# Kernel optimization log

Measured on AMD Instinct MI355X. Metric: run time of the kernel, lower is better.

Reference implementation:

```python
import jax, jax.numpy as jnp
import numpy as np

NG, NPG, EPG = 64, 256, 2048        # graphs, nodes/graph, edges/graph
N, E = NG * NPG, NG * EPG
FN, FE, FG = 256, 64, 128           # node/edge/global feature dims
MSG_DIMS = [FE + 2 * FN + FG, 512, 512, 256]   # message_arch '512-512-256'
UPD_DIMS = [256 + FN + FG, 512, 256]           # node_arch '512-256'
N_EMB_G, OUT_NODE, OUT_ACT = 256, 64, 8


def _mlp(x, params):
    # Linear -> ReLU stack (Dropout is identity in eval mode)
    for w, b in params:
        x = jax.nn.relu(x @ w + b)
    return x


def setup_inputs():
    key = jax.random.key(0)
    ks = jax.random.split(key, 24)
    nodes = jax.random.normal(ks[0], (N, FN), jnp.float32)
    edge_attr = jax.random.normal(ks[1], (E, FE), jnp.float32)
    global_attr = jax.random.normal(ks[2], (NG, FG), jnp.float32)
    # edges are grouped by graph (matches repeat_interleave(global, num_edges))
    rng = np.random.default_rng(0)
    gid_e = np.repeat(np.arange(NG), EPG)
    src = gid_e * NPG + rng.integers(0, NPG, E)
    tgt = gid_e * NPG + rng.integers(0, NPG, E)
    edge_indices = jnp.asarray(np.stack([src, tgt]), jnp.int32)
    num_nodes = jnp.full((NG,), NPG, jnp.int32)
    num_edges = jnp.full((NG,), EPG, jnp.int32)
    batch_indices = jnp.asarray(np.repeat(np.arange(NG), NPG), jnp.int32)

    def lin(k, fi, fo):
        kw, kb = jax.random.split(k)
        lim = 1.0 / np.sqrt(fi)
        return (jax.random.uniform(kw, (fi, fo), jnp.float32, -lim, lim),
                jax.random.uniform(kb, (fo,), jnp.float32, -lim, lim))

    inp = dict(nodes=nodes, edge_attr=edge_attr, global_attr=global_attr,
               edge_indices=edge_indices, num_nodes=num_nodes,
               num_edges=num_edges, batch_indices=batch_indices)
    for i in range(3):
        w, b = lin(ks[3 + i], MSG_DIMS[i], MSG_DIMS[i + 1])
        inp[f'msg_w{i}'], inp[f'msg_b{i}'] = w, b
    for i in range(2):
        w, b = lin(ks[6 + i], UPD_DIMS[i], UPD_DIMS[i + 1])
        inp[f'upd_w{i}'], inp[f'upd_b{i}'] = w, b
    inp['glob_w'], inp['glob_b'] = lin(ks[8], UPD_DIMS[-1] + FG, N_EMB_G)
    inp['emb_w'], inp['emb_b'] = lin(ks[9], UPD_DIMS[-1], OUT_NODE)
    inp['act_w'], inp['act_b'] = lin(ks[10], N_EMB_G, OUT_ACT)
    return inp


def reference(nodes, edge_attr, global_attr, edge_indices, num_nodes,
              num_edges, batch_indices, msg_w0, msg_b0, msg_w1, msg_b1,
              msg_w2, msg_b2, upd_w0, upd_b0, upd_w1, upd_b1,
              glob_w, glob_b, emb_w, emb_b, act_w, act_b):
    n, e = nodes.shape[0], edge_indices.shape[1]
    ng = global_attr.shape[0]
    src, tgt = edge_indices[0], edge_indices[1]
    glob_e = jnp.repeat(global_attr, num_edges, axis=0, total_repeat_length=e)
    concat = jnp.concatenate([nodes[src], edge_attr, nodes[tgt], glob_e], axis=1)
    # message_nn ends with ReLU; outer F.relu is a no-op on non-neg values
    message = _mlp(concat, [(msg_w0, msg_b0), (msg_w1, msg_b1), (msg_w2, msg_b2)])
    # scatter_max into per-node slots; messages >= 0 so zeros init matches fill=0
    aggr = jnp.zeros((n, message.shape[1]), message.dtype).at[tgt].max(message)
    glob_n = jnp.repeat(global_attr, num_nodes, axis=0, total_repeat_length=n)
    h = _mlp(jnp.concatenate([nodes, aggr, glob_n], axis=1),
             [(upd_w0, upd_b0), (upd_w1, upd_b1)])
    agg_nodes = jnp.zeros((ng, h.shape[1]), h.dtype).at[batch_indices].max(h)
    g = jax.nn.relu(jnp.concatenate([agg_nodes, global_attr], axis=1) @ glob_w + glob_b)
    node_pred = jax.nn.relu(h @ emb_w + emb_b)
    action = jax.nn.softmax(g @ act_w + act_b, axis=1)
    return node_pred, action
```

## Files before the change

kernel.cpp:

```cpp
#include <hip/hip_runtime.h>
#include <hip/hip_bf16.h>

typedef unsigned short u16;
using u16x4 = __attribute__((ext_vector_type(4))) unsigned short;
using u16x8 = __attribute__((ext_vector_type(8))) unsigned short;
using u32x4 = __attribute__((ext_vector_type(4))) unsigned int;
using f32x4 = __attribute__((ext_vector_type(4))) float;
using bf16x8 = __attribute__((ext_vector_type(8))) __bf16;

#define TNG 64
#define TNN 16384
#define TNE 131072
#define TFN 256
#define TFE 64
#define TFG 128

__device__ __forceinline__ u16 f2bf(float f) {
    unsigned u = __float_as_uint(f);
    unsigned r = (u + 0x7FFFu + ((u >> 16) & 1u)) >> 16;
    return (u16)r;
}
__device__ __forceinline__ float b2f(u16 h) {
    return __uint_as_float(((unsigned)h) << 16);
}

__device__ __forceinline__ void gload_lds16(const u16* g, u16* l) {
    __builtin_amdgcn_global_load_lds(
        (const __attribute__((address_space(1))) void*)g,
        (__attribute__((address_space(3))) void*)l, 16, 0, 0);
}

__device__ __forceinline__ int xcd_swz(int bid, int nwg) {
    return (nwg & 7) == 0 ? (bid & 7) * (nwg >> 3) + (bid >> 3) : bid;
}


__global__ void cast_kernel(const float* __restrict__ in, u16* __restrict__ out, int n4) {
    int i = blockIdx.x * 256 + threadIdx.x;
    if (i >= n4) return;
    f32x4 v = *(const f32x4*)(in + (size_t)i * 4);
    u16x4 o;
    o.x = f2bf(v.x); o.y = f2bf(v.y); o.z = f2bf(v.z); o.w = f2bf(v.w);
    *(u16x4*)(out + (size_t)i * 4) = o;
}


struct PrepTab {
    const float* W[8];
    int out_off[8];
    int Nin[8], Nact[8], r0[8], Ksub[8];
    int tile0[8];
    int tkn[8];
};

__global__ __launch_bounds__(256) void prep_weights_kernel(PrepTab tab, u16* __restrict__ wsbase) {
    const int b = blockIdx.x;
    int i = 7;
#pragma unroll
    for (int j = 7; j > 0; --j)
        if (b < tab.tile0[j]) i = j - 1;
    const int loc = b - tab.tile0[i];
    const int tk = loc % tab.tkn[i];
    const int tn = loc / tab.tkn[i];
    const int kb = tk * 64, nb = tn * 64;
    const int Nin = tab.Nin[i], Nact = tab.Nact[i], r0 = tab.r0[i], Ksub = tab.Ksub[i];
    const float* W = tab.W[i];
    u16* outp = wsbase + tab.out_off[i];

    __shared__ float t[64][65];
    const int tid = threadIdx.x;
    const int nl = tid & 63;
    const bool nok = (nb + nl) < Nact;
#pragma unroll 4
    for (int kk = tid >> 6; kk < 64; kk += 4) {
        float v = nok ? W[(size_t)(r0 + kb + kk) * Nin + nb + nl] : 0.0f;
        t[kk][nl] = v;
    }
    __syncthreads();
    const int kl = tid & 63;
#pragma unroll 4
    for (int nn = tid >> 6; nn < 64; nn += 4)
        outp[(size_t)(nb + nn) * Ksub + kb + kl] = f2bf(t[kl][nn]);
}


template <int K, int NXSH, bool RELU, bool OUT_BF16>
__global__ __launch_bounds__(256) void gemm_bt_kernel(
    const u16* __restrict__ A, const u16* __restrict__ Bt,
    const float* __restrict__ bias, void* __restrict__ Cv,
    int Nout, int ldc) {
    constexpr int NT = K / 32;
    __shared__ u16 As[3][4096];
    __shared__ u16 Bs[3][4096];
    const int w = xcd_swz(blockIdx.x, gridDim.x);
    const int bxi = w & ((1 << NXSH) - 1);
    const int byi = w >> NXSH;
    const int tid = threadIdx.x;
    const int wave = tid >> 6, lane = tid & 63;
    const int wr = wave >> 1, wc = wave & 1;
    const size_t brow = (size_t)byi * 128;
    const size_t bcol = (size_t)bxi * 128;
    const int srow = tid >> 2;
    const int qsrc = (tid & 3) ^ ((srow >> 1) & 3);
    const u16* aSrc = A + (brow + srow) * (size_t)K + qsrc * 8;
    const u16* bSrc = Bt + (bcol + srow) * (size_t)K + qsrc * 8;
    const size_t stepRows = (size_t)64 * K;

    auto stage = [&](int t, int buf) {
        const int k0 = t * 32;
        gload_lds16(aSrc + k0, &As[buf][tid * 8]);
        gload_lds16(aSrc + stepRows + k0, &As[buf][tid * 8 + 2048]);
        gload_lds16(bSrc + k0, &Bs[buf][tid * 8]);
        gload_lds16(bSrc + stepRows + k0, &Bs[buf][tid * 8 + 2048]);
    };

    f32x4 acc[4][4] = {};

    stage(0, 0);
    stage(1, 1);
#pragma unroll
    for (int t = 0; t < NT; ++t) {
        const int cur = t % 3;
        if (t + 1 < NT) asm volatile("s_waitcnt vmcnt(4)" ::: "memory");
        else            asm volatile("s_waitcnt vmcnt(0)" ::: "memory");
        __builtin_amdgcn_s_barrier();
        if (t + 2 < NT) stage(t + 2, (t + 2) % 3);
        bf16x8 af[4], bfv[4];
#pragma unroll
        for (int m = 0; m < 4; ++m) {
            const int row = wr * 64 + m * 16 + (lane & 15);
            const int slot = (lane >> 4) ^ ((row >> 1) & 3);
            af[m] = *(const bf16x8*)&As[cur][row * 32 + slot * 8];
        }
#pragma unroll
        for (int n = 0; n < 4; ++n) {
            const int row = wc * 64 + n * 16 + (lane & 15);
            const int slot = (lane >> 4) ^ ((row >> 1) & 3);
            bfv[n] = *(const bf16x8*)&Bs[cur][row * 32 + slot * 8];
        }
#pragma unroll
        for (int m = 0; m < 4; ++m)
#pragma unroll
            for (int n = 0; n < 4; ++n)
                acc[m][n] = __builtin_amdgcn_mfma_f32_16x16x32_bf16(af[m], bfv[n], acc[m][n], 0, 0, 0);
    }

    const int rowSub = wr * 64 + (lane >> 4) * 4;
#pragma unroll
    for (int n = 0; n < 4; ++n) {
        const int col = (int)bcol + wc * 64 + n * 16 + (lane & 15);
        if (col >= Nout) continue;
        const float bv = bias ? bias[col] : 0.0f;
#pragma unroll
        for (int m = 0; m < 4; ++m) {
#pragma unroll
            for (int i = 0; i < 4; ++i) {
                float v = acc[m][n][i] + bv;
                if (RELU) v = fmaxf(v, 0.0f);
                size_t off = (brow + rowSub + m * 16 + i) * (size_t)ldc + col;
                if (OUT_BF16) ((u16*)Cv)[off] = f2bf(v);
                else ((float*)Cv)[off] = v;
            }
        }
    }
}


__global__ __launch_bounds__(256) void gemm_u0_kernel(
    const u16* __restrict__ nodes_bf, const u16* __restrict__ aggr,
    const u16* __restrict__ glob_bf, const u16* __restrict__ U0T,
    const float* __restrict__ bias, u16* __restrict__ C) {
    constexpr int NT = 20;
    __shared__ u16 As[3][4096];
    __shared__ u16 Bs[3][4096];
    const int w = xcd_swz(blockIdx.x, gridDim.x);
    const int bxi = w & 3;
    const int byi = w >> 2;
    const int tid = threadIdx.x;
    const int wave = tid >> 6, lane = tid & 63;
    const int wr = wave >> 1, wc = wave & 1;
    const size_t brow = (size_t)byi * 128;
    const size_t bcol = (size_t)bxi * 128;
    const int srow = tid >> 2;
    const int scol = ((tid & 3) ^ ((srow >> 1) & 3)) * 8;
    const int r0i = (int)brow + srow;
    const u16* bSrc = U0T + (bcol + srow) * (size_t)640 + scol;

    auto stage = [&](int t, int buf) {
        const int k0 = t * 32;
        const u16 *p0, *p1;
        if (k0 < 256) {
            p0 = nodes_bf + (size_t)r0i * 256 + k0 + scol;
            p1 = nodes_bf + (size_t)(r0i + 64) * 256 + k0 + scol;
        } else if (k0 < 512) {
            p0 = aggr + (size_t)r0i * 256 + (k0 - 256) + scol;
            p1 = aggr + (size_t)(r0i + 64) * 256 + (k0 - 256) + scol;
        } else {
            p0 = glob_bf + (size_t)(r0i >> 8) * 128 + (k0 - 512) + scol;
            p1 = glob_bf + (size_t)((r0i + 64) >> 8) * 128 + (k0 - 512) + scol;
        }
        gload_lds16(p0, &As[buf][tid * 8]);
        gload_lds16(p1, &As[buf][tid * 8 + 2048]);
        gload_lds16(bSrc + k0, &Bs[buf][tid * 8]);
        gload_lds16(bSrc + (size_t)64 * 640 + k0, &Bs[buf][tid * 8 + 2048]);
    };

    f32x4 acc[4][4] = {};

    stage(0, 0);
    stage(1, 1);
#pragma unroll
    for (int t = 0; t < NT; ++t) {
        const int cur = t % 3;
        if (t + 1 < NT) asm volatile("s_waitcnt vmcnt(4)" ::: "memory");
        else            asm volatile("s_waitcnt vmcnt(0)" ::: "memory");
        __builtin_amdgcn_s_barrier();
        if (t + 2 < NT) stage(t + 2, (t + 2) % 3);
        bf16x8 af[4], bfv[4];
#pragma unroll
        for (int m = 0; m < 4; ++m) {
            const int row = wr * 64 + m * 16 + (lane & 15);
            const int slot = (lane >> 4) ^ ((row >> 1) & 3);
            af[m] = *(const bf16x8*)&As[cur][row * 32 + slot * 8];
        }
#pragma unroll
        for (int n = 0; n < 4; ++n) {
            const int row = wc * 64 + n * 16 + (lane & 15);
            const int slot = (lane >> 4) ^ ((row >> 1) & 3);
            bfv[n] = *(const bf16x8*)&Bs[cur][row * 32 + slot * 8];
        }
#pragma unroll
        for (int m = 0; m < 4; ++m)
#pragma unroll
            for (int n = 0; n < 4; ++n)
                acc[m][n] = __builtin_amdgcn_mfma_f32_16x16x32_bf16(af[m], bfv[n], acc[m][n], 0, 0, 0);
    }

    const int rowSub = wr * 64 + (lane >> 4) * 4;
#pragma unroll
    for (int n = 0; n < 4; ++n) {
        const int col = (int)bcol + wc * 64 + n * 16 + (lane & 15);
        const float bv = bias[col];
#pragma unroll
        for (int m = 0; m < 4; ++m)
#pragma unroll
            for (int i = 0; i < 4; ++i) {
                float v = fmaxf(acc[m][n][i] + bv, 0.0f);
                C[(brow + rowSub + m * 16 + i) * (size_t)512 + col] = f2bf(v);
            }
    }
}


__global__ __launch_bounds__(256) void gd_kernel(const float* __restrict__ glob,
                                                 const float* __restrict__ msg_w0,
                                                 const float* __restrict__ b0,
                                                 float* __restrict__ Gdb,
                                                 u16* __restrict__ glob_bf) {
    int g = blockIdx.x;
    __shared__ float in[TFG];
    if (threadIdx.x < TFG) {
        float v = glob[g * TFG + threadIdx.x];
        in[threadIdx.x] = v;
        glob_bf[g * TFG + threadIdx.x] = f2bf(v);
    }
    __syncthreads();
    for (int j = threadIdx.x; j < 512; j += 256) {
        float s = b0[j];
        for (int k = 0; k < TFG; ++k) s += in[k] * msg_w0[(size_t)(576 + k) * 512 + j];
        Gdb[(size_t)g * 512 + j] = s;
    }
}


__global__ __launch_bounds__(256) void h1_fused_kernel(
    const float* __restrict__ Ef, const u16* __restrict__ WbT,
    const u16* __restrict__ Pac, const float* __restrict__ Gdb,
    const int* __restrict__ src, const int* __restrict__ tgt,
    u16* __restrict__ h1, int e0) {
    __shared__ u16 smem[17408];
    u16* As = smem;
    u16* Bs = smem + 8192;
    const int w = xcd_swz(blockIdx.x, gridDim.x);
    const int bxi = w & 3;
    const int byi = w >> 2;
    const int tid = threadIdx.x;
    const int wave = tid >> 6, lane = tid & 63;
    const int wr = wave >> 1, wc = wave & 1;
    const int brow = byi * 128;
    const int bcol = bxi * 128;

    {
        const int r = tid >> 2;
        const int cq = (tid & 3) * 2;
        const int sw = r & 7;
#pragma unroll
        for (int h = 0; h < 2; ++h) {
            const float* sp = Ef + (size_t)(e0 + brow + r + h * 64) * 64 + cq * 8;
            f32x4 v0 = *(const f32x4*)(sp);
            f32x4 v1 = *(const f32x4*)(sp + 4);
            f32x4 v2 = *(const f32x4*)(sp + 8);
            f32x4 v3 = *(const f32x4*)(sp + 12);
            u16x8 o0, o1;
            o0[0] = f2bf(v0.x); o0[1] = f2bf(v0.y); o0[2] = f2bf(v0.z); o0[3] = f2bf(v0.w);
            o0[4] = f2bf(v1.x); o0[5] = f2bf(v1.y); o0[6] = f2bf(v1.z); o0[7] = f2bf(v1.w);
            o1[0] = f2bf(v2.x); o1[1] = f2bf(v2.y); o1[2] = f2bf(v2.z); o1[3] = f2bf(v2.w);
            o1[4] = f2bf(v3.x); o1[5] = f2bf(v3.y); o1[6] = f2bf(v3.z); o1[7] = f2bf(v3.w);
            *(u16x8*)&As[(r + h * 64) * 64 + (cq ^ sw) * 8] = o0;
            *(u16x8*)&As[(r + h * 64) * 64 + ((cq + 1) ^ sw) * 8] = o1;
        }
#pragma unroll
        for (int j = 0; j < 4; ++j) {
            int li = j * 256 + tid;
            int row = li >> 3;
            int gslot = (li & 7) ^ (row & 7);
            gload_lds16(WbT + (size_t)(bcol + row) * 64 + gslot * 8, &Bs[li * 8]);
        }
    }
    __syncthreads();

    f32x4 acc[4][4] = {};
#pragma unroll
    for (int k0 = 0; k0 < 64; k0 += 32) {
        bf16x8 af[4], bv[4];
#pragma unroll
        for (int m = 0; m < 4; ++m) {
            const int row = wr * 64 + m * 16 + (lane & 15);
            const int slot = ((k0 >> 3) + (lane >> 4)) ^ (row & 7);
            af[m] = *(const bf16x8*)&As[row * 64 + slot * 8];
        }
#pragma unroll
        for (int n = 0; n < 4; ++n) {
            const int row = wc * 64 + n * 16 + (lane & 15);
            const int slot = ((k0 >> 3) + (lane >> 4)) ^ (row & 7);
            bv[n] = *(const bf16x8*)&Bs[row * 64 + slot * 8];
        }
#pragma unroll
        for (int m = 0; m < 4; ++m)
#pragma unroll
            for (int n = 0; n < 4; ++n)
                acc[m][n] = __builtin_amdgcn_mfma_f32_16x16x32_bf16(af[m], bv[n], acc[m][n], 0, 0, 0);
    }
    __syncthreads();

    const int rowSub = wr * 64 + (lane >> 4) * 4;
#pragma unroll
    for (int m = 0; m < 4; ++m)
#pragma unroll
        for (int n = 0; n < 4; ++n)
#pragma unroll
            for (int i = 0; i < 4; ++i)
                smem[(rowSub + m * 16 + i) * 136 + wc * 64 + n * 16 + (lane & 15)] =
                    f2bf(acc[m][n][i]);
    __syncthreads();

#pragma unroll
    for (int it = 0; it < 8; ++it) {
        int lin = it * 256 + tid;
        int r = lin >> 4;
        int q = (lin & 15) * 8;
        int e = e0 + brow + r;
        int s = src[e];
        int t = tgt[e];
        int g = e >> 11;
        int col = bcol + q;
        u16x8 pa = *(const u16x8*)(Pac + (size_t)s * 1024 + col);
        u16x8 pc = *(const u16x8*)(Pac + (size_t)t * 1024 + 512 + col);
        u16x8 eb = *(const u16x8*)&smem[r * 136 + q];
        f32x4 g0 = *(const f32x4*)(Gdb + (size_t)g * 512 + col);
        f32x4 g1 = *(const f32x4*)(Gdb + (size_t)g * 512 + col + 4);
        u16x8 o;
#pragma unroll
        for (int j = 0; j < 8; ++j) {
            float gd = (j < 4) ? g0[j] : g1[j - 4];
            float v = b2f(pa[j]) + b2f(pc[j]) + b2f(eb[j]) + gd;
            o[j] = f2bf(fmaxf(v, 0.0f));
        }
        *(u16x8*)(h1 + (size_t)(brow + r) * 512 + col) = o;
    }
}


__global__ __launch_bounds__(1024) void scatter_max_kernel(
    const u16* __restrict__ msg, const int* __restrict__ tgt,
    u16* __restrict__ aggr) {
    int g = blockIdx.x >> 2;
    int fc = blockIdx.x & 3;
    __shared__ unsigned smax[256 * 64];
    int tid = threadIdx.x;
    for (int i = tid; i < 256 * 64; i += 1024) smax[i] = 0u;
    __syncthreads();
    const int eg = g * 2048;
    const int n0 = g * 256;
    const int f4 = (tid & 15) * 4;
    const int elane = tid >> 4;
    const u16* mbase = msg + fc * 64 + f4;
#pragma unroll
    for (int wv = 0; wv < 32; wv += 4) {
        const int e = eg + elane + wv * 64;
        int t0 = tgt[e], t1 = tgt[e + 64], t2 = tgt[e + 128], t3 = tgt[e + 192];
        u16x4 m0 = *(const u16x4*)(mbase + (size_t)e * 256);
        u16x4 m1 = *(const u16x4*)(mbase + (size_t)(e + 64) * 256);
        u16x4 m2 = *(const u16x4*)(mbase + (size_t)(e + 128) * 256);
        u16x4 m3 = *(const u16x4*)(mbase + (size_t)(e + 192) * 256);
        int a0 = t0 - n0, a1 = t1 - n0, a2 = t2 - n0, a3 = t3 - n0;
        if ((unsigned)a0 < 256u) {
            atomicMax(&smax[a0 * 64 + f4],     ((unsigned)m0.x) << 16);
            atomicMax(&smax[a0 * 64 + f4 + 1], ((unsigned)m0.y) << 16);
            atomicMax(&smax[a0 * 64 + f4 + 2], ((unsigned)m0.z) << 16);
            atomicMax(&smax[a0 * 64 + f4 + 3], ((unsigned)m0.w) << 16);
        }
        if ((unsigned)a1 < 256u) {
            atomicMax(&smax[a1 * 64 + f4],     ((unsigned)m1.x) << 16);
            atomicMax(&smax[a1 * 64 + f4 + 1], ((unsigned)m1.y) << 16);
            atomicMax(&smax[a1 * 64 + f4 + 2], ((unsigned)m1.z) << 16);
            atomicMax(&smax[a1 * 64 + f4 + 3], ((unsigned)m1.w) << 16);
        }
        if ((unsigned)a2 < 256u) {
            atomicMax(&smax[a2 * 64 + f4],     ((unsigned)m2.x) << 16);
            atomicMax(&smax[a2 * 64 + f4 + 1], ((unsigned)m2.y) << 16);
            atomicMax(&smax[a2 * 64 + f4 + 2], ((unsigned)m2.z) << 16);
            atomicMax(&smax[a2 * 64 + f4 + 3], ((unsigned)m2.w) << 16);
        }
        if ((unsigned)a3 < 256u) {
            atomicMax(&smax[a3 * 64 + f4],     ((unsigned)m3.x) << 16);
            atomicMax(&smax[a3 * 64 + f4 + 1], ((unsigned)m3.y) << 16);
            atomicMax(&smax[a3 * 64 + f4 + 2], ((unsigned)m3.z) << 16);
            atomicMax(&smax[a3 * 64 + f4 + 3], ((unsigned)m3.w) << 16);
        }
    }
    __syncthreads();
    for (int i = tid; i < 256 * 64; i += 1024) {
        int nl = i >> 6, ff = i & 63;
        aggr[(size_t)(n0 + nl) * 256 + fc * 64 + ff] = (u16)(smax[nl * 64 + ff] >> 16);
    }
}


__global__ __launch_bounds__(256) void head_kernel(
    const u16* __restrict__ h, const float* __restrict__ glob,
    const float* __restrict__ W, const float* __restrict__ b,
    const float* __restrict__ actw, const float* __restrict__ actb,
    float* __restrict__ out_act) {
    int g = blockIdx.x;
    int tid = threadIdx.x;
    __shared__ float in[384];
    __shared__ float go[256];
    __shared__ float logits[8];
    {
        const size_t base = (size_t)g * 256 * 256 + tid;
        float m0 = 0.0f, m1 = 0.0f, m2 = 0.0f, m3 = 0.0f;
        for (int n = 0; n < 256; n += 4) {
            m0 = fmaxf(m0, b2f(h[base + (size_t)n * 256]));
            m1 = fmaxf(m1, b2f(h[base + (size_t)(n + 1) * 256]));
            m2 = fmaxf(m2, b2f(h[base + (size_t)(n + 2) * 256]));
            m3 = fmaxf(m3, b2f(h[base + (size_t)(n + 3) * 256]));
        }
        in[tid] = fmaxf(fmaxf(m0, m1), fmaxf(m2, m3));
        if (tid < 128) in[256 + tid] = glob[(size_t)g * 128 + tid];
    }
    __syncthreads();
    {
        float s = b[tid];
        for (int k = 0; k < 384; ++k) s += in[k] * W[(size_t)k * 256 + tid];
        go[tid] = fmaxf(s, 0.0f);
    }
    __syncthreads();
    if (tid < 8) {
        float s = actb[tid];
        for (int k = 0; k < 256; ++k) s += go[k] * actw[(size_t)k * 8 + tid];
        logits[tid] = s;
    }
    __syncthreads();
    if (tid == 0) {
        float mx = logits[0];
        for (int i = 1; i < 8; ++i) mx = fmaxf(mx, logits[i]);
        float ex[8], den = 0.0f;
        for (int i = 0; i < 8; ++i) { ex[i] = expf(logits[i] - mx); den += ex[i]; }
        float inv = 1.0f / den;
        for (int i = 0; i < 8; ++i) out_act[(size_t)g * 8 + i] = ex[i] * inv;
    }
}


constexpr size_t OFF_NODES_BF = 0;
constexpr size_t OFF_GLOB_BF  = OFF_NODES_BF + (size_t)TNN * TFN * 2;
constexpr size_t OFF_WACT = OFF_GLOB_BF + (size_t)TNG * TFG * 2;
constexpr size_t OFF_WBT  = OFF_WACT + 1024 * 256 * 2;
constexpr size_t OFF_W1T  = OFF_WBT + 512 * 64 * 2;
constexpr size_t OFF_W2T  = OFF_W1T + 512 * 512 * 2;
constexpr size_t OFF_U0T  = OFF_W2T + 256 * 512 * 2;
constexpr size_t OFF_U1T  = OFF_U0T + 512 * 640 * 2;
constexpr size_t OFF_EMBT = OFF_U1T + 256 * 512 * 2;
constexpr size_t OFF_AGGR = OFF_EMBT + 128 * 256 * 2;
constexpr size_t OFF_GDB  = OFF_AGGR + (size_t)TNN * 256 * 2;
constexpr size_t OFF_PAC  = OFF_GDB + 64 * 512 * 4;
constexpr size_t OFF_MSG  = OFF_PAC + (size_t)TNN * 1024 * 2;
constexpr size_t OFF_V    = OFF_MSG + (size_t)TNE * 256 * 2;
constexpr size_t SZ_HU1   = (size_t)TNN * 512 * 2;

extern "C" void kernel_launch(void* const* d_in, const int* in_sizes, int n_in,
                              void* d_out, int out_size, void* d_ws, size_t ws_size,
                              hipStream_t stream) {
    const float* nodes       = (const float*)d_in[0];
    const float* edge_attr   = (const float*)d_in[1];
    const float* global_attr = (const float*)d_in[2];
    const int*   edge_idx    = (const int*)d_in[3];
    const float* msg_w0 = (const float*)d_in[7];
    const float* msg_b0 = (const float*)d_in[8];
    const float* msg_w1 = (const float*)d_in[9];
    const float* msg_b1 = (const float*)d_in[10];
    const float* msg_w2 = (const float*)d_in[11];
    const float* msg_b2 = (const float*)d_in[12];
    const float* upd_w0 = (const float*)d_in[13];
    const float* upd_b0 = (const float*)d_in[14];
    const float* upd_w1 = (const float*)d_in[15];
    const float* upd_b1 = (const float*)d_in[16];
    const float* glob_w = (const float*)d_in[17];
    const float* glob_b = (const float*)d_in[18];
    const float* emb_w  = (const float*)d_in[19];
    const float* emb_b  = (const float*)d_in[20];
    const float* act_w  = (const float*)d_in[21];
    const float* act_b  = (const float*)d_in[22];

    const int* src = edge_idx;
    const int* tgt = edge_idx + TNE;

    char* ws = (char*)d_ws;
    u16* nodes_bf = (u16*)(ws + OFF_NODES_BF);
    u16* glob_bf  = (u16*)(ws + OFF_GLOB_BF);
    u16* WacT = (u16*)(ws + OFF_WACT);
    u16* WbT  = (u16*)(ws + OFF_WBT);
    u16* W1T  = (u16*)(ws + OFF_W1T);
    u16* W2T  = (u16*)(ws + OFF_W2T);
    u16* U0T  = (u16*)(ws + OFF_U0T);
    u16* U1T  = (u16*)(ws + OFF_U1T);
    u16* EmbT = (u16*)(ws + OFF_EMBT);
    u16* aggr = (u16*)(ws + OFF_AGGR);
    float* Gdb = (float*)(ws + OFF_GDB);
    u16* Pac  = (u16*)(ws + OFF_PAC);
    u16* msgc = (u16*)(ws + OFF_MSG);
    float* out = (float*)d_out;

    size_t CH = 32768;
    while (CH > 2048 && OFF_V + CH * 2048 > ws_size) CH >>= 1;
    const int nchunk = (int)((size_t)TNE / CH);

    u16* h1c  = (u16*)(ws + OFF_V);
    u16* h2c  = (u16*)(ws + OFF_V + CH * 1024);
    u16* hu1  = (u16*)(ws + OFF_V);
    u16* h_bf = (u16*)(ws + OFF_AGGR);

    cast_kernel<<<(TNN * TFN / 4 + 255) / 256, 256, 0, stream>>>(nodes, nodes_bf, TNN * TFN / 4);

    PrepTab tab;
    int ntiles = 0;
    {
        const float* Ws[8]  = {msg_w0, msg_w0, msg_w0, msg_w1, msg_w2, upd_w0, upd_w1, emb_w};
        int offs[8] = {(int)(OFF_WACT / 2), (int)(OFF_WACT / 2) + 131072, (int)(OFF_WBT / 2),
                       (int)(OFF_W1T / 2), (int)(OFF_W2T / 2), (int)(OFF_U0T / 2),
                       (int)(OFF_U1T / 2), (int)(OFF_EMBT / 2)};
        int nin[8]  = {512, 512, 512, 512, 256, 512, 256, 64};
        int nact[8] = {512, 512, 512, 512, 256, 512, 256, 64};
        int r0v[8]  = {0, 320, 256, 0, 0, 0, 0, 0};
        int ksub[8] = {256, 256, 64, 512, 512, 640, 512, 256};
        int npad[8] = {512, 512, 512, 512, 256, 512, 256, 128};
        int acc = 0;
        for (int i = 0; i < 8; ++i) {
            tab.W[i] = Ws[i]; tab.out_off[i] = offs[i]; tab.Nin[i] = nin[i];
            tab.Nact[i] = nact[i]; tab.r0[i] = r0v[i]; tab.Ksub[i] = ksub[i];
            tab.tkn[i] = ksub[i] / 64;
            tab.tile0[i] = acc;
            acc += (npad[i] / 64) * (ksub[i] / 64);
        }
        ntiles = acc;
    }
    prep_weights_kernel<<<ntiles, 256, 0, stream>>>(tab, (u16*)ws);
    gd_kernel<<<64, 256, 0, stream>>>(global_attr, msg_w0, msg_b0, Gdb, glob_bf);

    gemm_bt_kernel<256, 3, false, true><<<1024, 256, 0, stream>>>(nodes_bf, WacT, nullptr, Pac, 1024, 1024);

    for (int ci = 0; ci < nchunk; ++ci) {
        const int e0 = (int)(ci * CH);
        const int nwg = (int)(CH / 32);
        h1_fused_kernel<<<nwg, 256, 0, stream>>>(
            edge_attr, WbT, Pac, Gdb, src, tgt, h1c, e0);
        gemm_bt_kernel<512, 2, true, true><<<nwg, 256, 0, stream>>>(h1c, W1T, msg_b1, h2c, 512, 512);
        gemm_bt_kernel<512, 1, true, true><<<nwg / 2, 256, 0, stream>>>(
            h2c, W2T, msg_b2, msgc + (size_t)e0 * 256, 256, 256);
    }
    scatter_max_kernel<<<TNG * 4, 1024, 0, stream>>>(msgc, tgt, aggr);

    gemm_u0_kernel<<<512, 256, 0, stream>>>(nodes_bf, aggr, glob_bf, U0T, upd_b0, hu1);
    gemm_bt_kernel<512, 1, true, true><<<256, 256, 0, stream>>>(hu1, U1T, upd_b1, h_bf, 256, 256);

    head_kernel<<<64, 256, 0, stream>>>(h_bf, global_attr, glob_w, glob_b,
                                        act_w, act_b, out + (size_t)TNN * 64);
    gemm_bt_kernel<256, 0, true, false><<<128, 256, 0, stream>>>(h_bf, EmbT, emb_b, out, 64, 64);

    (void)in_sizes; (void)n_in; (void)out_size;
}
```

Measured before the change: 348.7 us.

## Load GEMM B operand directly into registers instead of staging through LDS

In both GEMM kernels the weight (B) tiles are no longer staged through shared memory. Each wave now loads its own B fragments straight from global memory into double-buffered registers, and the vmcnt wait threshold is adjusted to match. This halves LDS use and removes the B-side LDS reads, with the aim of raising occupancy and cutting LDS traffic. The cost is redundant global loads of B across the two wave rows, less coalesced per-lane loads, and extra register pressure. The vmcnt ordering also depends on how the compiler schedules the loads.

```diff
diff --git a/kernel.cpp b/kernel.cpp
--- a/kernel.cpp
+++ b/kernel.cpp
@@ -91,7 +91,6 @@
     int Nout, int ldc) {
     constexpr int NT = K / 32;
     __shared__ u16 As[3][4096];
-    __shared__ u16 Bs[3][4096];
     const int w = xcd_swz(blockIdx.x, gridDim.x);
     const int bxi = w & ((1 << NXSH) - 1);
     const int byi = w >> NXSH;
@@ -103,40 +102,56 @@
     const int srow = tid >> 2;
     const int qsrc = (tid & 3) ^ ((srow >> 1) & 3);
     const u16* aSrc = A + (brow + srow) * (size_t)K + qsrc * 8;
-    const u16* bSrc = Bt + (bcol + srow) * (size_t)K + qsrc * 8;
     const size_t stepRows = (size_t)64 * K;
 
-    auto stage = [&](int t, int buf) {
+    const u16* bp0 = Bt + (size_t)(bcol + wc * 64 + 0 * 16 + (lane & 15)) * K + (lane >> 4) * 8;
+    const u16* bp1 = Bt + (size_t)(bcol + wc * 64 + 1 * 16 + (lane & 15)) * K + (lane >> 4) * 8;
+    const u16* bp2 = Bt + (size_t)(bcol + wc * 64 + 2 * 16 + (lane & 15)) * K + (lane >> 4) * 8;
+    const u16* bp3 = Bt + (size_t)(bcol + wc * 64 + 3 * 16 + (lane & 15)) * K + (lane >> 4) * 8;
+
+    auto stageA = [&](int t, int buf) {
         const int k0 = t * 32;
         gload_lds16(aSrc + k0, &As[buf][tid * 8]);
         gload_lds16(aSrc + stepRows + k0, &As[buf][tid * 8 + 2048]);
-        gload_lds16(bSrc + k0, &Bs[buf][tid * 8]);
-        gload_lds16(bSrc + stepRows + k0, &Bs[buf][tid * 8 + 2048]);
     };
 
     f32x4 acc[4][4] = {};
-
-    stage(0, 0);
-    stage(1, 1);
+    u32x4 breg[2][4];
+
+    stageA(0, 0);
+    breg[0][0] = *(const u32x4*)(bp0);
+    breg[0][1] = *(const u32x4*)(bp1);
+    breg[0][2] = *(const u32x4*)(bp2);
+    breg[0][3] = *(const u32x4*)(bp3);
+    stageA(1, 1);
+    breg[1][0] = *(const u32x4*)(bp0 + 32);
+    breg[1][1] = *(const u32x4*)(bp1 + 32);
+    breg[1][2] = *(const u32x4*)(bp2 + 32);
+    breg[1][3] = *(const u32x4*)(bp3 + 32);
+
 #pragma unroll
     for (int t = 0; t < NT; ++t) {
         const int cur = t % 3;
-        if (t + 1 < NT) asm volatile("s_waitcnt vmcnt(4)" ::: "memory");
+        if (t + 1 < NT) asm volatile("s_waitcnt vmcnt(6)" ::: "memory");
         else            asm volatile("s_waitcnt vmcnt(0)" ::: "memory");
         __builtin_amdgcn_s_barrier();
-        if (t + 2 < NT) stage(t + 2, (t + 2) % 3);
-        bf16x8 af[4], bfv[4];
+        bf16x8 bfv[4];
+#pragma unroll
+        for (int n = 0; n < 4; ++n)
+            bfv[n] = __builtin_bit_cast(bf16x8, breg[t & 1][n]);
+        if (t + 2 < NT) {
+            stageA(t + 2, (t + 2) % 3);
+            breg[t & 1][0] = *(const u32x4*)(bp0 + (t + 2) * 32);
+            breg[t & 1][1] = *(const u32x4*)(bp1 + (t + 2) * 32);
+            breg[t & 1][2] = *(const u32x4*)(bp2 + (t + 2) * 32);
+            breg[t & 1][3] = *(const u32x4*)(bp3 + (t + 2) * 32);
+        }
+        bf16x8 af[4];
 #pragma unroll
         for (int m = 0; m < 4; ++m) {
             const int row = wr * 64 + m * 16 + (lane & 15);
             const int slot = (lane >> 4) ^ ((row >> 1) & 3);
             af[m] = *(const bf16x8*)&As[cur][row * 32 + slot * 8];
-        }
-#pragma unroll
-        for (int n = 0; n < 4; ++n) {
-            const int row = wc * 64 + n * 16 + (lane & 15);
-            const int slot = (lane >> 4) ^ ((row >> 1) & 3);
-            bfv[n] = *(const bf16x8*)&Bs[cur][row * 32 + slot * 8];
         }
 #pragma unroll
         for (int m = 0; m < 4; ++m)
@@ -172,7 +187,6 @@
     const float* __restrict__ bias, u16* __restrict__ C) {
     constexpr int NT = 20;
     __shared__ u16 As[3][4096];
-    __shared__ u16 Bs[3][4096];
     const int w = xcd_swz(blockIdx.x, gridDim.x);
     const int bxi = w & 3;
     const int byi = w >> 2;
@@ -184,9 +198,13 @@
     const int srow = tid >> 2;
     const int scol = ((tid & 3) ^ ((srow >> 1) & 3)) * 8;
     const int r0i = (int)brow + srow;
-    const u16* bSrc = U0T + (bcol + srow) * (size_t)640 + scol;
-
-    auto stage = [&](int t, int buf) {
+
+    const u16* bp0 = U0T + (size_t)(bcol + wc * 64 + 0 * 16 + (lane & 15)) * 640 + (lane >> 4) * 8;
+    const u16* bp1 = U0T + (size_t)(bcol + wc * 64 + 1 * 16 + (lane & 15)) * 640 + (lane >> 4) * 8;
+    const u16* bp2 = U0T + (size_t)(bcol + wc * 64 + 2 * 16 + (lane & 15)) * 640 + (lane >> 4) * 8;
+    const u16* bp3 = U0T + (size_t)(bcol + wc * 64 + 3 * 16 + (lane & 15)) * 640 + (lane >> 4) * 8;
+
+    auto stageA = [&](int t, int buf) {
         const int k0 = t * 32;
         const u16 *p0, *p1;
         if (k0 < 256) {
@@ -201,33 +219,45 @@
         }
         gload_lds16(p0, &As[buf][tid * 8]);
         gload_lds16(p1, &As[buf][tid * 8 + 2048]);
-        gload_lds16(bSrc + k0, &Bs[buf][tid * 8]);
-        gload_lds16(bSrc + (size_t)64 * 640 + k0, &Bs[buf][tid * 8 + 2048]);
     };
 
     f32x4 acc[4][4] = {};
-
-    stage(0, 0);
-    stage(1, 1);
+    u32x4 breg[2][4];
+
+    stageA(0, 0);
+    breg[0][0] = *(const u32x4*)(bp0);
+    breg[0][1] = *(const u32x4*)(bp1);
+    breg[0][2] = *(const u32x4*)(bp2);
+    breg[0][3] = *(const u32x4*)(bp3);
+    stageA(1, 1);
+    breg[1][0] = *(const u32x4*)(bp0 + 32);
+    breg[1][1] = *(const u32x4*)(bp1 + 32);
+    breg[1][2] = *(const u32x4*)(bp2 + 32);
+    breg[1][3] = *(const u32x4*)(bp3 + 32);
+
 #pragma unroll
     for (int t = 0; t < NT; ++t) {
         const int cur = t % 3;
-        if (t + 1 < NT) asm volatile("s_waitcnt vmcnt(4)" ::: "memory");
+        if (t + 1 < NT) asm volatile("s_waitcnt vmcnt(6)" ::: "memory");
         else            asm volatile("s_waitcnt vmcnt(0)" ::: "memory");
         __builtin_amdgcn_s_barrier();
-        if (t + 2 < NT) stage(t + 2, (t + 2) % 3);
-        bf16x8 af[4], bfv[4];
+        bf16x8 bfv[4];
+#pragma unroll
+        for (int n = 0; n < 4; ++n)
+            bfv[n] = __builtin_bit_cast(bf16x8, breg[t & 1][n]);
+        if (t + 2 < NT) {
+            stageA(t + 2, (t + 2) % 3);
+            breg[t & 1][0] = *(const u32x4*)(bp0 + (t + 2) * 32);
+            breg[t & 1][1] = *(const u32x4*)(bp1 + (t + 2) * 32);
+            breg[t & 1][2] = *(const u32x4*)(bp2 + (t + 2) * 32);
+            breg[t & 1][3] = *(const u32x4*)(bp3 + (t + 2) * 32);
+        }
+        bf16x8 af[4];
 #pragma unroll
         for (int m = 0; m < 4; ++m) {
             const int row = wr * 64 + m * 16 + (lane & 15);
             const int slot = (lane >> 4) ^ ((row >> 1) & 3);
             af[m] = *(const bf16x8*)&As[cur][row * 32 + slot * 8];
-        }
-#pragma unroll
-        for (int n = 0; n < 4; ++n) {
-            const int row = wc * 64 + n * 16 + (lane & 15);
-            const int slot = (lane >> 4) ^ ((row >> 1) & 3);
-            bfv[n] = *(const bf16x8*)&Bs[cur][row * 32 + slot * 8];
         }
 #pragma unroll
         for (int m = 0; m < 4; ++m)
```

New measurement: 459.9 us. 1.32x slower.
